# Kernel tuning notes

Hardware: AMD Instinct MI355X
Metric: run time of the kernel (lower is better)

Reference implementation:

```python
import jax, jax.numpy as jnp
import numpy as np

IGNORE = 0  # ignore label (default in LovaszSoftmax.__init__)


def setup_inputs() -> dict:
    key = jax.random.key(0)
    k1, k2 = jax.random.split(key)
    B, C, H, W = 4, 20, 512, 1024
    logits = jax.random.normal(k1, (B, C, H, W), dtype=jnp.float32)
    labels = jax.random.randint(k2, (B, H, W), 0, 20, dtype=jnp.int32)
    return {"logits": logits, "labels": labels}


def _lovasz_softmax(logits, labels, ignore=IGNORE):
    # logits: [B,C,H,W], labels: [B,H,W]
    B, C, H, W = logits.shape
    probas = jax.nn.softmax(logits, axis=1)
    pf = probas.transpose(0, 2, 3, 1).reshape(-1, C)  # [N, C]
    lf = labels.reshape(-1)                            # [N]
    valid = lf != ignore                               # [N]

    def per_class(c):
        # Ignored pixels get fg=0 and pred=0 -> error 0, so they sort to the
        # tail and contribute 0 to the dot product (equivalent to filtering
        # them out, but jit-compatible with static shapes).
        fg = ((lf == c) & valid).astype(pf.dtype)      # [N]
        pred = jnp.where(valid, pf[:, c], 0.0)         # [N]
        errors = jnp.abs(fg - pred)
        order = jnp.argsort(-errors)                   # descending sort perm
        errors_sorted = errors[order]
        fg_sorted = fg[order]
        # Lovasz gradient of sorted ground truth
        gts = fg_sorted.sum()
        intersection = gts - jnp.cumsum(fg_sorted)
        union = gts + jnp.cumsum(1.0 - fg_sorted)
        jaccard = 1.0 - intersection / union
        jaccard = jnp.concatenate([jaccard[:1], jaccard[1:] - jaccard[:-1]])
        loss_c = jnp.dot(errors_sorted, jaccard)
        present = fg.sum() > 0                          # classes='present'
        return loss_c, present

    losses, present = jax.vmap(per_class)(jnp.arange(C))
    p = present.astype(losses.dtype)
    # mean over present classes (matches 'present' + mean() in torch source)
    return jnp.sum(losses * p) / jnp.maximum(jnp.sum(p), 1.0)


def reference(logits, labels):
    return _lovasz_softmax(logits, labels, IGNORE)
```

## Files before the change

kernel.cpp:

```cpp
#include <hip/hip_runtime.h>

#define NCLS 20
#define NBIN 192
#define RREP 2
#define HWSZ (512*1024)
#define NPIX (4*HWSZ)
#define NBLKH 256
#define NTHRH 512
#define NSWP 8
#define SGRP 4

__global__ __launch_bounds__(NTHRH)
void hist_kernel(const float* __restrict__ logits,
                 const int* __restrict__ labels,
                 unsigned int* __restrict__ bhist)
{
    __shared__ unsigned int lh[NCLS * NBIN * RREP];
    for (int i = threadIdx.x; i < NCLS * NBIN * RREP; i += NTHRH) lh[i] = 0u;
    __syncthreads();

    const int r = threadIdx.x & (RREP - 1);

#pragma unroll
    for (int s = 0; s < NSWP; s++) {
        const int pp = (s * NBLKH + blockIdx.x) * NTHRH + threadIdx.x;
        const int n  = pp << 1;
        const int b  = n >> 19;
        const int hw = n & (HWSZ - 1);
        const float2* base =
            (const float2*)(logits + (size_t)b * NCLS * HWSZ + hw);

        float2 x[NCLS];
        float Z0 = 0.f, Z1 = 0.f;
#pragma unroll
        for (int c = 0; c < NCLS; c++) {
            float2 v = base[c * (HWSZ / 2)];
            v.x = __expf(v.x);
            v.y = __expf(v.y);
            Z0 += v.x;
            Z1 += v.y;
            x[c] = v;
        }
        const float invZ0 = 1.f / Z0;
        const float invZ1 = 1.f / Z1;

        const int2 lv = ((const int2*)labels)[pp];
        const bool v0 = (lv.x != 0), v1 = (lv.y != 0);

#pragma unroll
        for (int c = 0; c < NCLS; c++) {
            const float p0 = x[c].x * invZ0;
            const float p1 = x[c].y * invZ1;
            const bool f0 = v0 && (lv.x == c);
            const bool f1 = v1 && (lv.y == c);
            const float e0 = v0 ? (f0 ? 1.f - p0 : p0) : 0.f;
            const float e1 = v1 ? (f1 ? 1.f - p1 : p1) : 0.f;
            int b0 = (int)(e0 * (float)NBIN); b0 = b0 > NBIN-1 ? NBIN-1 : b0;
            int b1 = (int)(e1 * (float)NBIN); b1 = b1 > NBIN-1 ? NBIN-1 : b1;
            unsigned q0 = f0 ? 0x10001u : 1u;
            unsigned q1 = f1 ? 0x10001u : 1u;
            if (b0 == b1) { q0 += q1; q1 = 0u; }
            if (!(b0 == 0 && q0 < 0x10000u))
                atomicAdd(&lh[(c * NBIN + b0) * RREP + r], q0);
            if (q1 && !(b1 == 0 && q1 < 0x10000u))
                atomicAdd(&lh[(c * NBIN + b1) * RREP + r], q1);
        }
    }
    __syncthreads();

    unsigned int* out = bhist + (size_t)blockIdx.x * (NCLS * NBIN);
    for (int i = threadIdx.x; i < NCLS * NBIN; i += NTHRH) {
        out[i] = lh[i * RREP + 0] + lh[i * RREP + 1];
    }
}

__global__ void scan_kernel(const unsigned int* __restrict__ bhist,
                            float* __restrict__ cls)
{
    __shared__ float pcnt[SGRP][NBIN];
    __shared__ float pfg[SGRP][NBIN];
    __shared__ float scnt[NBIN];
    __shared__ float sfg[NBIN];
    __shared__ float stot;

    const int c = blockIdx.x;
    const int t = threadIdx.x;
    const int g = t / NBIN;
    const int bin = t - g * NBIN;

    unsigned int cnt = 0, fg = 0;
    for (int b = g * (NBLKH / SGRP); b < (g + 1) * (NBLKH / SGRP); b++) {
        const unsigned int v = bhist[(size_t)b * (NCLS * NBIN) + c * NBIN + bin];
        cnt += v & 0xFFFFu;
        fg  += v >> 16;
    }
    pcnt[g][bin] = (float)cnt;
    pfg[g][bin]  = (float)fg;
    __syncthreads();

    if (t < NBIN) {
        scnt[t] = pcnt[0][t] + pcnt[1][t] + pcnt[2][t] + pcnt[3][t];
        sfg[t]  = pfg[0][t]  + pfg[1][t]  + pfg[2][t]  + pfg[3][t];
    }
    __syncthreads();

    if (t < 64) {
        float tot = 0.f;
        for (int j = t; j < NBIN; j += 64) tot += scnt[j];
        for (int off = 32; off; off >>= 1) tot += __shfl_down(tot, off);
        if (t == 0) stot = tot;
    }
    __syncthreads();
    if (t == 0) scnt[0] += (float)NPIX - stot;
    __syncthreads();

    if (t < 64) {
        const int lane = t;
        float fgsum = 0.f;
        for (int j = lane; j < NBIN; j += 64) fgsum += sfg[j];
        for (int off = 32; off; off >>= 1) fgsum += __shfl_down(fgsum, off);
        const float gts = __shfl(fgsum, 0);

        float loss = 0.f;
        if (gts > 0.f) {
            float Tc = 0.f, Fc = 0.f, acc = 0.f;
            for (int chunk = 0; chunk < NBIN / 64; chunk++) {
                const int k = NBIN - 1 - (chunk * 64 + lane);
                float ci = scnt[k];
                float fi = sfg[k];
                const float cnt_k = ci, fg_k = fi;
                for (int off = 1; off < 64; off <<= 1) {
                    const float cu = __shfl_up(ci, off);
                    const float fu = __shfl_up(fi, off);
                    if (lane >= off) { ci += cu; fi += fu; }
                }
                const float T1 = Tc + ci, F1 = Fc + fi;
                const float T0 = T1 - cnt_k, F0 = F1 - fg_k;

                const float J1 = 1.f - (gts - F1) / (gts + T1 - F1);
                const float J0 = 1.f - (gts - F0) / (gts + T0 - F0);
                const float center = ((float)k + 0.5f) * (1.0f / (float)NBIN);
                acc += center * (J1 - J0);

                Tc = __shfl(T1, 63);
                Fc = __shfl(F1, 63);
            }
            for (int off = 32; off; off >>= 1) acc += __shfl_down(acc, off);
            loss = acc;
        }
        if (lane == 0) {
            cls[c]        = loss;
            cls[NCLS + c] = (gts > 0.f) ? 1.f : 0.f;
        }
    }
}

__global__ void finalize_kernel(const float* __restrict__ cls,
                                float* __restrict__ out)
{
    if (threadIdx.x == 0 && blockIdx.x == 0) {
        float sl = 0.f, sp = 0.f;
        for (int c = 0; c < NCLS; c++) {
            sl += cls[c] * cls[NCLS + c];
            sp += cls[NCLS + c];
        }
        out[0] = sl / fmaxf(sp, 1.f);
    }
}

extern "C" void kernel_launch(void* const* d_in, const int* in_sizes, int n_in,
                              void* d_out, int out_size, void* d_ws, size_t ws_size,
                              hipStream_t stream)
{
    const float* logits = (const float*)d_in[0];
    const int*   labels = (const int*)d_in[1];

    unsigned int* bhist = (unsigned int*)d_ws;
    float* cls = (float*)((char*)d_ws + (size_t)NBLKH * NCLS * NBIN * 4);

    hist_kernel<<<NBLKH, NTHRH, 0, stream>>>(logits, labels, bhist);
    scan_kernel<<<NCLS, SGRP * NBIN, 0, stream>>>(bhist, cls);
    finalize_kernel<<<1, 1, 0, stream>>>(cls, (float*)d_out);
}
```

Baseline: 252.6 us.

## Process four pixels per thread with float4 loads and fold finalize into scan

After: 261.2 us. 1.03x slower.

```diff
diff --git a/kernel.cpp b/kernel.cpp
--- a/kernel.cpp
+++ b/kernel.cpp
@@ -5,16 +5,25 @@
 #define RREP 2
 #define HWSZ (512*1024)
 #define NPIX (4*HWSZ)
-#define NBLKH 256
-#define NTHRH 512
-#define NSWP 8
+#define NBLKH 512
+#define NTHRH 256
+#define NSWP 4
 #define SGRP 4
+
+#define ACC_OFF ((size_t)NBLKH * NCLS * NBIN)
 
 __global__ __launch_bounds__(NTHRH)
 void hist_kernel(const float* __restrict__ logits,
                  const int* __restrict__ labels,
                  unsigned int* __restrict__ bhist)
 {
+    if (blockIdx.x == 0 && threadIdx.x == 0) {
+        float* acc = (float*)(bhist + ACC_OFF);
+        acc[0] = 0.f;
+        acc[1] = 0.f;
+        ((unsigned int*)acc)[2] = 0u;
+    }
+
     __shared__ unsigned int lh[NCLS * NBIN * RREP];
     for (int i = threadIdx.x; i < NCLS * NBIN * RREP; i += NTHRH) lh[i] = 0u;
     __syncthreads();
@@ -23,47 +32,63 @@
 
 #pragma unroll
     for (int s = 0; s < NSWP; s++) {
-        const int pp = (s * NBLKH + blockIdx.x) * NTHRH + threadIdx.x;
-        const int n  = pp << 1;
+        const int qq = (s * NBLKH + blockIdx.x) * NTHRH + threadIdx.x;
+        const int n  = qq << 2;
         const int b  = n >> 19;
         const int hw = n & (HWSZ - 1);
-        const float2* base =
-            (const float2*)(logits + (size_t)b * NCLS * HWSZ + hw);
-
-        float2 x[NCLS];
-        float Z0 = 0.f, Z1 = 0.f;
+        const float4* base =
+            (const float4*)(logits + (size_t)b * NCLS * HWSZ + hw);
+
+        float4 x[NCLS];
+        float Z0 = 0.f, Z1 = 0.f, Z2 = 0.f, Z3 = 0.f;
 #pragma unroll
         for (int c = 0; c < NCLS; c++) {
-            float2 v = base[c * (HWSZ / 2)];
-            v.x = __expf(v.x);
-            v.y = __expf(v.y);
-            Z0 += v.x;
-            Z1 += v.y;
+            float4 v = base[c * (HWSZ / 4)];
+            v.x = __expf(v.x); v.y = __expf(v.y);
+            v.z = __expf(v.z); v.w = __expf(v.w);
+            Z0 += v.x; Z1 += v.y; Z2 += v.z; Z3 += v.w;
             x[c] = v;
         }
-        const float invZ0 = 1.f / Z0;
-        const float invZ1 = 1.f / Z1;
-
-        const int2 lv = ((const int2*)labels)[pp];
+        const float i0 = 1.f / Z0, i1 = 1.f / Z1;
+        const float i2 = 1.f / Z2, i3 = 1.f / Z3;
+
+        const int4 lv = ((const int4*)labels)[qq];
         const bool v0 = (lv.x != 0), v1 = (lv.y != 0);
+        const bool v2 = (lv.z != 0), v3 = (lv.w != 0);
 
 #pragma unroll
         for (int c = 0; c < NCLS; c++) {
-            const float p0 = x[c].x * invZ0;
-            const float p1 = x[c].y * invZ1;
             const bool f0 = v0 && (lv.x == c);
             const bool f1 = v1 && (lv.y == c);
-            const float e0 = v0 ? (f0 ? 1.f - p0 : p0) : 0.f;
-            const float e1 = v1 ? (f1 ? 1.f - p1 : p1) : 0.f;
+            const bool f2 = v2 && (lv.z == c);
+            const bool f3 = v3 && (lv.w == c);
+            const float e0 = v0 ? (f0 ? 1.f - x[c].x * i0 : x[c].x * i0) : 0.f;
+            const float e1 = v1 ? (f1 ? 1.f - x[c].y * i1 : x[c].y * i1) : 0.f;
+            const float e2 = v2 ? (f2 ? 1.f - x[c].z * i2 : x[c].z * i2) : 0.f;
+            const float e3 = v3 ? (f3 ? 1.f - x[c].w * i3 : x[c].w * i3) : 0.f;
             int b0 = (int)(e0 * (float)NBIN); b0 = b0 > NBIN-1 ? NBIN-1 : b0;
             int b1 = (int)(e1 * (float)NBIN); b1 = b1 > NBIN-1 ? NBIN-1 : b1;
+            int b2 = (int)(e2 * (float)NBIN); b2 = b2 > NBIN-1 ? NBIN-1 : b2;
+            int b3 = (int)(e3 * (float)NBIN); b3 = b3 > NBIN-1 ? NBIN-1 : b3;
             unsigned q0 = f0 ? 0x10001u : 1u;
             unsigned q1 = f1 ? 0x10001u : 1u;
-            if (b0 == b1) { q0 += q1; q1 = 0u; }
-            if (!(b0 == 0 && q0 < 0x10000u))
+            unsigned q2 = f2 ? 0x10001u : 1u;
+            unsigned q3 = f3 ? 0x10001u : 1u;
+            if (b1 == b0) { q0 += q1; q1 = 0u; }
+            if (b3 == b2) { q2 += q3; q3 = 0u; }
+            if (b2 == b0) { q0 += q2; q2 = 0u; }
+            if (q3) {
+                if      (b3 == b0) { q0 += q3; q3 = 0u; }
+                else if (b3 == b1) { q1 += q3; q3 = 0u; }
+            }
+            if (q0 && !(b0 == 0 && q0 < 0x10000u))
                 atomicAdd(&lh[(c * NBIN + b0) * RREP + r], q0);
             if (q1 && !(b1 == 0 && q1 < 0x10000u))
                 atomicAdd(&lh[(c * NBIN + b1) * RREP + r], q1);
+            if (q2 && !(b2 == 0 && q2 < 0x10000u))
+                atomicAdd(&lh[(c * NBIN + b2) * RREP + r], q2);
+            if (q3 && !(b3 == 0 && q3 < 0x10000u))
+                atomicAdd(&lh[(c * NBIN + b3) * RREP + r], q3);
         }
     }
     __syncthreads();
@@ -75,7 +100,7 @@
 }
 
 __global__ void scan_kernel(const unsigned int* __restrict__ bhist,
-                            float* __restrict__ cls)
+                            float* __restrict__ dout)
 {
     __shared__ float pcnt[SGRP][NBIN];
     __shared__ float pfg[SGRP][NBIN];
@@ -83,6 +108,9 @@
     __shared__ float sfg[NBIN];
     __shared__ float stot;
 
+    float* acc = (float*)(bhist + ACC_OFF);
+    unsigned int* ticket = (unsigned int*)acc + 2;
+
     const int c = blockIdx.x;
     const int t = threadIdx.x;
     const int g = t / NBIN;
@@ -123,7 +151,7 @@
 
         float loss = 0.f;
         if (gts > 0.f) {
-            float Tc = 0.f, Fc = 0.f, acc = 0.f;
+            float Tc = 0.f, Fc = 0.f, a = 0.f;
             for (int chunk = 0; chunk < NBIN / 64; chunk++) {
                 const int k = NBIN - 1 - (chunk * 64 + lane);
                 float ci = scnt[k];
@@ -140,31 +168,27 @@
                 const float J1 = 1.f - (gts - F1) / (gts + T1 - F1);
                 const float J0 = 1.f - (gts - F0) / (gts + T0 - F0);
                 const float center = ((float)k + 0.5f) * (1.0f / (float)NBIN);
-                acc += center * (J1 - J0);
+                a += center * (J1 - J0);
 
                 Tc = __shfl(T1, 63);
                 Fc = __shfl(F1, 63);
             }
-            for (int off = 32; off; off >>= 1) acc += __shfl_down(acc, off);
-            loss = acc;
-        }
+            for (int off = 32; off; off >>= 1) a += __shfl_down(a, off);
+            loss = a;
+        }
+
         if (lane == 0) {
-            cls[c]        = loss;
-            cls[NCLS + c] = (gts > 0.f) ? 1.f : 0.f;
-        }
-    }
-}
-
-__global__ void finalize_kernel(const float* __restrict__ cls,
-                                float* __restrict__ out)
-{
-    if (threadIdx.x == 0 && blockIdx.x == 0) {
-        float sl = 0.f, sp = 0.f;
-        for (int c = 0; c < NCLS; c++) {
-            sl += cls[c] * cls[NCLS + c];
-            sp += cls[NCLS + c];
-        }
-        out[0] = sl / fmaxf(sp, 1.f);
+            const float present = (gts > 0.f) ? 1.f : 0.f;
+            atomicAdd(&acc[0], loss * present);
+            atomicAdd(&acc[1], present);
+            __threadfence();
+            const unsigned int done = atomicAdd(ticket, 1u);
+            if (done == NCLS - 1) {
+                const float sl = atomicAdd(&acc[0], 0.f);
+                const float sp = atomicAdd(&acc[1], 0.f);
+                dout[0] = sl / fmaxf(sp, 1.f);
+            }
+        }
     }
 }
 
@@ -176,9 +200,7 @@
     const int*   labels = (const int*)d_in[1];
 
     unsigned int* bhist = (unsigned int*)d_ws;
-    float* cls = (float*)((char*)d_ws + (size_t)NBLKH * NCLS * NBIN * 4);
 
     hist_kernel<<<NBLKH, NTHRH, 0, stream>>>(logits, labels, bhist);
-    scan_kernel<<<NCLS, SGRP * NBIN, 0, stream>>>(bhist, cls);
-    finalize_kernel<<<1, 1, 0, stream>>>(cls, (float*)d_out);
+    scan_kernel<<<NCLS, SGRP * NBIN, 0, stream>>>(bhist, (float*)d_out);
 }
```
